# Kernel tuning notes

Hardware: AMD Instinct MI355X
Metric: run time of the kernel (lower is better)

The kernel has to match this reference:

```python
import jax, jax.numpy as jnp
import numpy as np

EPS = 1e-5

def layernorm(x, g, b):
    mu = jnp.mean(x, axis=-1, keepdims=True)
    var = jnp.var(x, axis=-1, keepdims=True)
    return (x - mu) / jnp.sqrt(var + EPS) * g + b

def hpmlp(x, wa, ba, wb, bb):
    # Linear(in,H) -> GELU(erf) -> Linear(H,H); dropout is identity in eval
    h = jax.nn.gelu(x @ wa + ba, approximate=False)
    return h @ wb + bb

def setup_inputs() -> dict:
    key = jax.random.key(0)
    ks = jax.random.split(key, 8)
    B, S, H = 16, 4096, 768
    s = 0.02
    return {
        "tokens": jax.random.normal(ks[0], (B, S + 1, H), jnp.float32),
        "lengths": jax.random.randint(ks[1], (B,), 1, S + 1),
        "q": jax.random.normal(ks[2], (2, H), jnp.float32) * s,
        "ln_g": jnp.ones((H,), jnp.float32),
        "ln_b": jnp.zeros((H,), jnp.float32),
        "w1a": jax.random.normal(ks[3], (3 * H, H), jnp.float32) * s,
        "b1a": jnp.zeros((H,), jnp.float32),
        "w1b": jax.random.normal(ks[4], (H, H), jnp.float32) * s,
        "b1b": jnp.zeros((H,), jnp.float32),
        "w2a": jax.random.normal(ks[5], (3 * H, H), jnp.float32) * s,
        "b2a": jnp.zeros((H,), jnp.float32),
        "w2b": jax.random.normal(ks[6], (H, H), jnp.float32) * s,
        "b2b": jnp.zeros((H,), jnp.float32),
    }

def reference(tokens, lengths, q, ln_g, ln_b, w1a, b1a, w1b, b1b, w2a, b2a, w2b, b2b):
    clf = tokens[:, 0]          # [B, H]
    x = tokens[:, 1:]           # [B, S, H]
    B, S, H = x.shape
    mask = jnp.arange(S)[None, :] < lengths[:, None]      # [B, S]
    m3 = mask[..., None]
    denom = lengths.astype(x.dtype)[:, None]
    mean_pooled = jnp.sum(jnp.where(m3, x, 0.0), axis=1) / denom
    max_pooled = jnp.max(jnp.where(m3, x, -jnp.inf), axis=1)
    min_pooled = jnp.min(jnp.where(m3, x, jnp.inf), axis=1)
    # PatchMerger with 2 learned queries over length-masked tokens
    xn = layernorm(x, ln_g, ln_b)                          # [B, S, H]
    logits = jnp.einsum("qh,bsh->bqs", q, xn) * (H ** -0.5)
    logits = jnp.where(mask[:, None, :], logits, -jnp.inf)
    attn = jax.nn.softmax(logits, axis=-1)                 # [B, 2, S]
    pmp = jnp.einsum("bqs,bsh->bqh", attn, xn)             # [B, 2, H]
    pooled_trad = jnp.concatenate([mean_pooled, max_pooled, min_pooled], -1)  # [B, 3H]
    pooled_learn = jnp.concatenate([pmp.reshape(B, 2 * H), clf], -1)          # [B, 3H]
    return jnp.concatenate([
        hpmlp(pooled_trad, w1a, b1a, w1b, b1b),
        hpmlp(pooled_learn, w2a, b2a, w2b, b2b),
    ], -1)
```

## Files before the change

kernel.cpp:

```cpp
#include <hip/hip_runtime.h>
#include <cmath>
#include <cstddef>

#define HD    768
#define BATCH 16
#define SROW  4097
#define NCH   64
#define CS    64
#define TPW   16
#define REC   3856
#define NK1   72
#define K1SEG 32
#define NK2   24
#define K2SEG 32
#define QSCALE 0.03608439182435161f

__device__ inline void wred4(float& a, float& b, float& c, float& d) {
#pragma unroll
  for (int off = 32; off > 0; off >>= 1) {
    a += __shfl_xor(a, off, 64);
    b += __shfl_xor(b, off, 64);
    c += __shfl_xor(c, off, 64);
    d += __shfl_xor(d, off, 64);
  }
}

__global__ __launch_bounds__(256, 3) void k1_pass(
    const float* __restrict__ tokens, const int* __restrict__ lengths,
    const float* __restrict__ q, const float* __restrict__ ln_g,
    const float* __restrict__ ln_b, float* __restrict__ rec)
{
  const int b = blockIdx.y, c = blockIdx.x;
  const int tid = threadIdx.x, w = tid >> 6, lane = tid & 63;
  const int len = lengths[b];
  if (c * CS >= len) return;

  float gq0[12], gq1[12];
  float G0 = 0.f, G1 = 0.f, C0 = 0.f, C1 = 0.f;
#pragma unroll
  for (int e = 0; e < 3; ++e) {
    const int off = e * 256 + lane * 4;
    const float4 qa = *(const float4*)(q + off);
    const float4 qb = *(const float4*)(q + HD + off);
    const float4 gg = *(const float4*)(ln_g + off);
    const float4 bb = *(const float4*)(ln_b + off);
    const float qav[4] = {qa.x, qa.y, qa.z, qa.w};
    const float qbv[4] = {qb.x, qb.y, qb.z, qb.w};
    const float ggv[4] = {gg.x, gg.y, gg.z, gg.w};
    const float bbv[4] = {bb.x, bb.y, bb.z, bb.w};
#pragma unroll
    for (int j = 0; j < 4; ++j) {
      const float g0 = ggv[j] * qav[j] * QSCALE;
      const float g1 = ggv[j] * qbv[j] * QSCALE;
      gq0[e * 4 + j] = g0;  gq1[e * 4 + j] = g1;
      G0 += g0;  G1 += g1;
      C0 = fmaf(bbv[j] * QSCALE, qav[j], C0);
      C1 = fmaf(bbv[j] * QSCALE, qbv[j], C1);
    }
  }
  wred4(G0, G1, C0, C1);

  float psum[12], pmax[12], pmin[12], A0[12], A1[12];
#pragma unroll
  for (int i = 0; i < 12; ++i) {
    psum[i] = 0.f; pmax[i] = -INFINITY; pmin[i] = INFINITY;
    A0[i] = 0.f; A1[i] = 0.f;
  }
  float m0 = -INFINITY, l0 = 0.f, B0 = 0.f;
  float m1 = -INFINITY, l1 = 0.f, B1 = 0.f;

  const int sbase = c * CS + w * TPW;
  const int rem0  = len - sbase;
  const int nt    = rem0 < 0 ? 0 : (rem0 < TPW ? rem0 : TPW);

  const float* xr = tokens + ((size_t)b * SROW + 1 + sbase) * HD + lane * 4;

  float4 nxa, nxb, nxc;
  if (nt > 0) {
    nxa = *(const float4*)(xr);
    nxb = *(const float4*)(xr + 256);
    nxc = *(const float4*)(xr + 512);
  }

  for (int t = 0; t < nt; ++t) {
    float xv[12];
    *(float4*)(xv)     = nxa;
    *(float4*)(xv + 4) = nxb;
    *(float4*)(xv + 8) = nxc;
    if (t + 1 < nt) {
      xr += HD;
      nxa = *(const float4*)(xr);
      nxb = *(const float4*)(xr + 256);
      nxc = *(const float4*)(xr + 512);
    }

    float s1 = 0.f, s2 = 0.f, dx0 = 0.f, dx1 = 0.f;
#pragma unroll
    for (int i = 0; i < 12; ++i) {
      s1 += xv[i];
      s2 = fmaf(xv[i], xv[i], s2);
      dx0 = fmaf(xv[i], gq0[i], dx0);
      dx1 = fmaf(xv[i], gq1[i], dx1);
    }
    wred4(s1, s2, dx0, dx1);
    const float mu   = s1 * (1.f / HD);
    const float var  = fmaf(-mu, mu, s2 * (1.f / HD));
    const float rstd = rsqrtf(var + 1e-5f);
    const float d0 = fmaf(rstd, fmaf(-mu, G0, dx0), C0);
    const float d1 = fmaf(rstd, fmaf(-mu, G1, dx1), C1);

    const float mn0 = fmaxf(m0, d0);
    const float al0 = __expf(m0 - mn0);
    const float p0  = __expf(d0 - mn0);
    const float c0  = p0 * rstd;
    l0 = fmaf(l0, al0, p0);  B0 = fmaf(B0, al0, c0 * mu);  m0 = mn0;

    const float mn1 = fmaxf(m1, d1);
    const float al1 = __expf(m1 - mn1);
    const float p1  = __expf(d1 - mn1);
    const float c1  = p1 * rstd;
    l1 = fmaf(l1, al1, p1);  B1 = fmaf(B1, al1, c1 * mu);  m1 = mn1;

#pragma unroll
    for (int i = 0; i < 12; ++i) {
      psum[i] += xv[i];
      pmax[i] = fmaxf(pmax[i], xv[i]);
      pmin[i] = fminf(pmin[i], xv[i]);
      A0[i] = fmaf(A0[i], al0, c0 * xv[i]);
      A1[i] = fmaf(A1[i], al1, c1 * xv[i]);
    }
  }

  __shared__ float ls[4][2][HD];
  __shared__ float lml[4][6];
#pragma unroll
  for (int e = 0; e < 3; ++e) {
    const int off = e * 256 + lane * 4;
    *(float4*)&ls[w][0][off] = *(const float4*)(psum + 4 * e);
    *(float4*)&ls[w][1][off] = *(const float4*)(pmax + 4 * e);
  }
  if (lane == 0) {
    lml[w][0] = m0; lml[w][1] = l0; lml[w][2] = B0;
    lml[w][3] = m1; lml[w][4] = l1; lml[w][5] = B1;
  }
  __syncthreads();

  float bm0 = -INFINITY, bm1 = -INFINITY;
#pragma unroll
  for (int wv = 0; wv < 4; ++wv) {
    bm0 = fmaxf(bm0, lml[wv][0]);
    bm1 = fmaxf(bm1, lml[wv][3]);
  }
  float sc0[4], sc1[4], bl0 = 0.f, bB0 = 0.f, bl1 = 0.f, bB1 = 0.f;
#pragma unroll
  for (int wv = 0; wv < 4; ++wv) {
    sc0[wv] = (lml[wv][1] > 0.f) ? __expf(lml[wv][0] - bm0) : 0.f;
    sc1[wv] = (lml[wv][4] > 0.f) ? __expf(lml[wv][3] - bm1) : 0.f;
    bl0 = fmaf(lml[wv][1], sc0[wv], bl0);  bB0 = fmaf(lml[wv][2], sc0[wv], bB0);
    bl1 = fmaf(lml[wv][4], sc1[wv], bl1);  bB1 = fmaf(lml[wv][5], sc1[wv], bB1);
  }

  float* r = rec + (size_t)(b * NCH + c) * REC;
#pragma unroll
  for (int e = 0; e < 3; ++e) {
    const int h = tid + 256 * e;
    float su = 0.f, mx = -INFINITY;
#pragma unroll
    for (int wv = 0; wv < 4; ++wv) {
      su += ls[wv][0][h];
      mx = fmaxf(mx, ls[wv][1][h]);
    }
    r[h] = su;  r[HD + h] = mx;
  }
  __syncthreads();
#pragma unroll
  for (int e = 0; e < 3; ++e) {
    const int off = e * 256 + lane * 4;
    *(float4*)&ls[w][0][off] = *(const float4*)(pmin + 4 * e);
    *(float4*)&ls[w][1][off] = *(const float4*)(A0 + 4 * e);
  }
  __syncthreads();
#pragma unroll
  for (int e = 0; e < 3; ++e) {
    const int h = tid + 256 * e;
    float mn_ = INFINITY, a0 = 0.f;
#pragma unroll
    for (int wv = 0; wv < 4; ++wv) {
      mn_ = fminf(mn_, ls[wv][0][h]);
      a0 = fmaf(ls[wv][1][h], sc0[wv], a0);
    }
    r[2 * HD + h] = mn_;  r[3 * HD + h] = a0;
  }
  __syncthreads();
#pragma unroll
  for (int e = 0; e < 3; ++e) {
    const int off = e * 256 + lane * 4;
    *(float4*)&ls[w][0][off] = *(const float4*)(A1 + 4 * e);
  }
  __syncthreads();
#pragma unroll
  for (int e = 0; e < 3; ++e) {
    const int h = tid + 256 * e;
    float a1 = 0.f;
#pragma unroll
    for (int wv = 0; wv < 4; ++wv) a1 = fmaf(ls[wv][0][h], sc1[wv], a1);
    r[4 * HD + h] = a1;
  }
  if (tid == 0) {
    r[3840] = bm0; r[3841] = bl0; r[3842] = bB0;
    r[3843] = bm1; r[3844] = bl1; r[3845] = bB1;
  }
}

__global__ __launch_bounds__(256) void k2_combine(
    const float* __restrict__ rec, const float* __restrict__ tokens,
    const int* __restrict__ lengths, const float* __restrict__ ln_g,
    const float* __restrict__ ln_b, const float* __restrict__ b1a,
    const float* __restrict__ b2a, const float* __restrict__ b1b,
    const float* __restrict__ b2b, float* __restrict__ pt,
    float* __restrict__ pl, float* __restrict__ hbuf,
    float* __restrict__ out)
{
  const int b = blockIdx.y, seg = blockIdx.x;
  const int tid = threadIdx.x, ln = tid & 63, cs = tid >> 6;
  const int h_ = seg * 64 + ln;
  const int len = lengths[b];
  const int nch = (len + CS - 1) / CS;
  const float* rb = rec + (size_t)b * NCH * REC;

  __shared__ float lmx[4][2];
  __shared__ float lsc[4][4];
  __shared__ float lbuf[5][4][64];

  float mq0 = -INFINITY, mq1 = -INFINITY;
  for (int cc = 0; cc < NCH / 4; ++cc) {
    const int c = cs * (NCH / 4) + cc;
    if (c >= nch) break;
    const float* rm = rb + (size_t)c * REC + 3840;
    mq0 = fmaxf(mq0, rm[0]);
    mq1 = fmaxf(mq1, rm[3]);
  }
  if (ln == 0) { lmx[cs][0] = mq0; lmx[cs][1] = mq1; }
  __syncthreads();
  const float mg0 = fmaxf(fmaxf(lmx[0][0], lmx[1][0]),
                          fmaxf(lmx[2][0], lmx[3][0]));
  const float mg1 = fmaxf(fmaxf(lmx[0][1], lmx[1][1]),
                          fmaxf(lmx[2][1], lmx[3][1]));

  float lg0 = 0.f, Bg0 = 0.f, lg1 = 0.f, Bg1 = 0.f;
  float S = 0.f, MX = -INFINITY, MN = INFINITY, A0 = 0.f, A1 = 0.f;
  for (int cc = 0; cc < NCH / 4; ++cc) {
    const int c = cs * (NCH / 4) + cc;
    if (c >= nch) break;
    const float* r = rb + (size_t)c * REC;
    const float e0 = __expf(r[3840] - mg0);
    const float e1 = __expf(r[3843] - mg1);
    lg0 = fmaf(r[3841], e0, lg0);  Bg0 = fmaf(r[3842], e0, Bg0);
    lg1 = fmaf(r[3844], e1, lg1);  Bg1 = fmaf(r[3845], e1, Bg1);
    S += r[h_];
    MX = fmaxf(MX, r[HD + h_]);
    MN = fminf(MN, r[2 * HD + h_]);
    A0 = fmaf(r[3 * HD + h_], e0, A0);
    A1 = fmaf(r[4 * HD + h_], e1, A1);
  }

  lbuf[0][cs][ln] = S;  lbuf[1][cs][ln] = MX; lbuf[2][cs][ln] = MN;
  lbuf[3][cs][ln] = A0; lbuf[4][cs][ln] = A1;
  if (ln == 0) {
    lsc[cs][0] = lg0; lsc[cs][1] = Bg0; lsc[cs][2] = lg1; lsc[cs][3] = Bg1;
  }
  __syncthreads();
  if (cs == 0) {
#pragma unroll
    for (int k = 1; k < 4; ++k) {
      S  += lbuf[0][k][ln];
      MX  = fmaxf(MX, lbuf[1][k][ln]);
      MN  = fminf(MN, lbuf[2][k][ln]);
      A0 += lbuf[3][k][ln];
      A1 += lbuf[4][k][ln];
    }
    const float Lg0 = lsc[0][0] + lsc[1][0] + lsc[2][0] + lsc[3][0];
    const float BG0 = lsc[0][1] + lsc[1][1] + lsc[2][1] + lsc[3][1];
    const float Lg1 = lsc[0][2] + lsc[1][2] + lsc[2][2] + lsc[3][2];
    const float BG1 = lsc[0][3] + lsc[1][3] + lsc[2][3] + lsc[3][3];
    const float invlen = 1.f / (float)len;
    const float il0 = 1.f / Lg0, il1 = 1.f / Lg1;
    const float gg = ln_g[h_], bb = ln_b[h_];
    float* ptb = pt + (size_t)b * 2304;
    float* plb = pl + (size_t)b * 2304;
    ptb[h_] = S * invlen;
    ptb[HD + h_] = MX;
    ptb[2 * HD + h_] = MN;
    plb[h_]      = fmaf(gg, (A0 - BG0) * il0, bb);
    plb[HD + h_] = fmaf(gg, (A1 - BG1) * il1, bb);
    plb[2 * HD + h_] = tokens[(size_t)b * SROW * HD + h_];
  }

  const int gidx = (b * 12 + seg) * 256 + tid;
  if (gidx < 2 * BATCH * HD) {
    const int j = gidx % HD, r2 = (gidx / HD) & 1;
    out[gidx] = (r2 ? b2b : b1b)[j];
  } else {
    const int g2 = gidx - 2 * BATCH * HD;
    const int j = g2 % HD;
    const int mlp = g2 / (BATCH * HD);
    hbuf[g2] = (mlp ? b2a : b1a)[j];
  }
}

__global__ __launch_bounds__(256) void k3_gemm1(
    const float* __restrict__ pt, const float* __restrict__ pl,
    const float* __restrict__ w1a, const float* __restrict__ w2a,
    float* __restrict__ hbuf)
{
  const int kseg = blockIdx.x, jseg = blockIdx.y, mlp = blockIdx.z;
  const int j = jseg * 256 + threadIdx.x;
  const float* xs = mlp ? pl : pt;
  const float* wA = mlp ? w2a : w1a;
  float acc[16];
#pragma unroll
  for (int bb = 0; bb < 16; ++bb) acc[bb] = 0.f;
  const int k0 = kseg * K1SEG;
#pragma unroll 4
  for (int kk = 0; kk < K1SEG; ++kk) {
    const int k = k0 + kk;
    const float wv = wA[(size_t)k * HD + j];
#pragma unroll
    for (int bb = 0; bb < 16; ++bb)
      acc[bb] = fmaf(xs[bb * 2304 + k], wv, acc[bb]);
  }
  float* hm = hbuf + (size_t)mlp * BATCH * HD;
#pragma unroll
  for (int bb = 0; bb < 16; ++bb)
    unsafeAtomicAdd(&hm[bb * HD + j], acc[bb]);
}

__global__ __launch_bounds__(256) void k4_gemm2(
    const float* __restrict__ hbuf, const float* __restrict__ w1b,
    const float* __restrict__ w2b, float* __restrict__ out)
{
  const int kseg = blockIdx.x, jseg = blockIdx.y, mlp = blockIdx.z;
  const int tid = threadIdx.x;
  const int j = jseg * 256 + tid;
  const int k0 = kseg * K2SEG;
  __shared__ float hs[16][K2SEG];

  const float* hm = hbuf + (size_t)mlp * BATCH * HD;
#pragma unroll
  for (int u = 0; u < (16 * K2SEG) / 256; ++u) {
    const int lin = tid + 256 * u;
    const int bb = lin / K2SEG, kk = lin % K2SEG;
    const float a = hm[bb * HD + k0 + kk];
    hs[bb][kk] = 0.5f * a * (1.f + erff(a * 0.70710678118654752f));
  }
  __syncthreads();

  const float* wB = mlp ? w2b : w1b;
  float acc2[16];
#pragma unroll
  for (int bb = 0; bb < 16; ++bb) acc2[bb] = 0.f;
#pragma unroll 4
  for (int kk = 0; kk < K2SEG; ++kk) {
    const float wv = wB[(size_t)(k0 + kk) * HD + j];
#pragma unroll
    for (int bb = 0; bb < 16; ++bb)
      acc2[bb] = fmaf(hs[bb][kk], wv, acc2[bb]);
  }
#pragma unroll
  for (int bb = 0; bb < 16; ++bb)
    unsafeAtomicAdd(&out[(size_t)bb * 1536 + mlp * HD + j], acc2[bb]);
}

extern "C" void kernel_launch(void* const* d_in, const int* in_sizes, int n_in,
                              void* d_out, int out_size, void* d_ws, size_t ws_size,
                              hipStream_t stream)
{
  const float* tokens = (const float*)d_in[0];
  const int*   lengths = (const int*)d_in[1];
  const float* q    = (const float*)d_in[2];
  const float* ln_g = (const float*)d_in[3];
  const float* ln_b = (const float*)d_in[4];
  const float* w1a  = (const float*)d_in[5];
  const float* b1a  = (const float*)d_in[6];
  const float* w1b  = (const float*)d_in[7];
  const float* b1b  = (const float*)d_in[8];
  const float* w2a  = (const float*)d_in[9];
  const float* b2a  = (const float*)d_in[10];
  const float* w2b  = (const float*)d_in[11];
  const float* b2b  = (const float*)d_in[12];
  float* out = (float*)d_out;

  float* ws   = (float*)d_ws;
  float* rec  = ws;
  float* pt   = rec + (size_t)BATCH * NCH * REC;
  float* pl   = pt + (size_t)BATCH * 2304;
  float* hbuf = pl + (size_t)BATCH * 2304;

  hipLaunchKernelGGL(k1_pass, dim3(NCH, BATCH), dim3(256), 0, stream,
                     tokens, lengths, q, ln_g, ln_b, rec);
  hipLaunchKernelGGL(k2_combine, dim3(12, BATCH), dim3(256), 0, stream,
                     rec, tokens, lengths, ln_g, ln_b, b1a, b2a, b1b, b2b,
                     pt, pl, hbuf, out);
  hipLaunchKernelGGL(k3_gemm1, dim3(NK1, 3, 2), dim3(256), 0, stream,
                     pt, pl, w1a, w2a, hbuf);
  hipLaunchKernelGGL(k4_gemm2, dim3(NK2, 3, 2), dim3(256), 0, stream,
                     hbuf, w1b, w2b, out);
}
```

Baseline: 310.0 us.

## Double-buffer token loads in pass kernel and preload weights in GEMV kernels

```diff
diff --git a/kernel.cpp b/kernel.cpp
--- a/kernel.cpp
+++ b/kernel.cpp
@@ -25,7 +25,7 @@
   }
 }
 
-__global__ __launch_bounds__(256, 3) void k1_pass(
+__global__ __launch_bounds__(256, 2) void k1_pass(
     const float* __restrict__ tokens, const int* __restrict__ lengths,
     const float* __restrict__ q, const float* __restrict__ ln_g,
     const float* __restrict__ ln_b, float* __restrict__ rec)
@@ -75,25 +75,7 @@
 
   const float* xr = tokens + ((size_t)b * SROW + 1 + sbase) * HD + lane * 4;
 
-  float4 nxa, nxb, nxc;
-  if (nt > 0) {
-    nxa = *(const float4*)(xr);
-    nxb = *(const float4*)(xr + 256);
-    nxc = *(const float4*)(xr + 512);
-  }
-
-  for (int t = 0; t < nt; ++t) {
-    float xv[12];
-    *(float4*)(xv)     = nxa;
-    *(float4*)(xv + 4) = nxb;
-    *(float4*)(xv + 8) = nxc;
-    if (t + 1 < nt) {
-      xr += HD;
-      nxa = *(const float4*)(xr);
-      nxb = *(const float4*)(xr + 256);
-      nxc = *(const float4*)(xr + 512);
-    }
-
+  auto token_body = [&](const float* xv) {
     float s1 = 0.f, s2 = 0.f, dx0 = 0.f, dx1 = 0.f;
 #pragma unroll
     for (int i = 0; i < 12; ++i) {
@@ -128,6 +110,58 @@
       pmin[i] = fminf(pmin[i], xv[i]);
       A0[i] = fmaf(A0[i], al0, c0 * xv[i]);
       A1[i] = fmaf(A1[i], al1, c1 * xv[i]);
+    }
+  };
+
+  if (nt == TPW) {
+    float4 pa0 = *(const float4*)(xr);
+    float4 pb0 = *(const float4*)(xr + 256);
+    float4 pc0 = *(const float4*)(xr + 512);
+    float4 pa1 = *(const float4*)(xr + HD);
+    float4 pb1 = *(const float4*)(xr + HD + 256);
+    float4 pc1 = *(const float4*)(xr + HD + 512);
+#pragma unroll
+    for (int t = 0; t < TPW; ++t) {
+      float xv[12];
+      if ((t & 1) == 0) {
+        *(float4*)(xv)     = pa0;
+        *(float4*)(xv + 4) = pb0;
+        *(float4*)(xv + 8) = pc0;
+        if (t + 2 < TPW) {
+          const float* xn_ = xr + (size_t)(t + 2) * HD;
+          pa0 = *(const float4*)(xn_);
+          pb0 = *(const float4*)(xn_ + 256);
+          pc0 = *(const float4*)(xn_ + 512);
+        }
+      } else {
+        *(float4*)(xv)     = pa1;
+        *(float4*)(xv + 4) = pb1;
+        *(float4*)(xv + 8) = pc1;
+        if (t + 2 < TPW) {
+          const float* xn_ = xr + (size_t)(t + 2) * HD;
+          pa1 = *(const float4*)(xn_);
+          pb1 = *(const float4*)(xn_ + 256);
+          pc1 = *(const float4*)(xn_ + 512);
+        }
+      }
+      token_body(xv);
+    }
+  } else if (nt > 0) {
+    float4 nxa = *(const float4*)(xr);
+    float4 nxb = *(const float4*)(xr + 256);
+    float4 nxc = *(const float4*)(xr + 512);
+    for (int t = 0; t < nt; ++t) {
+      float xv[12];
+      *(float4*)(xv)     = nxa;
+      *(float4*)(xv + 4) = nxb;
+      *(float4*)(xv + 8) = nxc;
+      if (t + 1 < nt) {
+        xr += HD;
+        nxa = *(const float4*)(xr);
+        nxb = *(const float4*)(xr + 256);
+        nxc = *(const float4*)(xr + 512);
+      }
+      token_body(xv);
     }
   }
 
@@ -317,18 +351,29 @@
   const int j = jseg * 256 + threadIdx.x;
   const float* xs = mlp ? pl : pt;
   const float* wA = mlp ? w2a : w1a;
+  const int k0 = kseg * K1SEG;
+
+  float wv[K1SEG];
+#pragma unroll
+  for (int kk = 0; kk < K1SEG; ++kk)
+    wv[kk] = wA[(size_t)(k0 + kk) * HD + j];
+
   float acc[16];
 #pragma unroll
-  for (int bb = 0; bb < 16; ++bb) acc[bb] = 0.f;
-  const int k0 = kseg * K1SEG;
-#pragma unroll 4
-  for (int kk = 0; kk < K1SEG; ++kk) {
-    const int k = k0 + kk;
-    const float wv = wA[(size_t)k * HD + j];
-#pragma unroll
-    for (int bb = 0; bb < 16; ++bb)
-      acc[bb] = fmaf(xs[bb * 2304 + k], wv, acc[bb]);
-  }
+  for (int bb = 0; bb < 16; ++bb) {
+    const float4* xp = (const float4*)(xs + bb * 2304 + k0);
+    float a = 0.f;
+#pragma unroll
+    for (int qq = 0; qq < K1SEG / 4; ++qq) {
+      const float4 xq = xp[qq];
+      a = fmaf(xq.x, wv[4 * qq + 0], a);
+      a = fmaf(xq.y, wv[4 * qq + 1], a);
+      a = fmaf(xq.z, wv[4 * qq + 2], a);
+      a = fmaf(xq.w, wv[4 * qq + 3], a);
+    }
+    acc[bb] = a;
+  }
+
   float* hm = hbuf + (size_t)mlp * BATCH * HD;
 #pragma unroll
   for (int bb = 0; bb < 16; ++bb)
@@ -345,6 +390,12 @@
   const int k0 = kseg * K2SEG;
   __shared__ float hs[16][K2SEG];
 
+  const float* wB = mlp ? w2b : w1b;
+  float wv[K2SEG];
+#pragma unroll
+  for (int kk = 0; kk < K2SEG; ++kk)
+    wv[kk] = wB[(size_t)(k0 + kk) * HD + j];
+
   const float* hm = hbuf + (size_t)mlp * BATCH * HD;
 #pragma unroll
   for (int u = 0; u < (16 * K2SEG) / 256; ++u) {
@@ -355,16 +406,14 @@
   }
   __syncthreads();
 
-  const float* wB = mlp ? w2b : w1b;
   float acc2[16];
 #pragma unroll
-  for (int bb = 0; bb < 16; ++bb) acc2[bb] = 0.f;
-#pragma unroll 4
-  for (int kk = 0; kk < K2SEG; ++kk) {
-    const float wv = wB[(size_t)(k0 + kk) * HD + j];
-#pragma unroll
-    for (int bb = 0; bb < 16; ++bb)
-      acc2[bb] = fmaf(hs[bb][kk], wv, acc2[bb]);
+  for (int bb = 0; bb < 16; ++bb) {
+    float a = 0.f;
+#pragma unroll
+    for (int kk = 0; kk < K2SEG; ++kk)
+      a = fmaf(hs[bb][kk], wv[kk], a);
+    acc2[bb] = a;
   }
 #pragma unroll
   for (int bb = 0; bb < 16; ++bb)
```

Result: slower. 340.7 us (+9.9%).
